# Performance work log

Measured on AMD Instinct MI355X. Metric: run time of the kernel, lower is better.

## Reference

```python
import jax, jax.numpy as jnp
import numpy as np

B, S, D_IN, D_OUT, H = 2, 2048, 1024, 1024, 16
HD = D_OUT // H


def setup_inputs() -> dict:
    key = jax.random.key(0)
    ks = jax.random.split(key, 6)
    x = jax.random.normal(ks[0], (B, S, D_IN), jnp.float32)
    Wq = jax.random.normal(ks[1], (D_IN, D_OUT), jnp.float32) * 0.02
    Wk = jax.random.normal(ks[2], (D_IN, D_OUT), jnp.float32) * 0.02
    Wv = jax.random.normal(ks[3], (D_IN, D_OUT), jnp.float32) * 0.02
    Wo = jax.random.normal(ks[4], (D_OUT, D_OUT), jnp.float32) * 0.02
    bo = jax.random.normal(ks[5], (D_OUT,), jnp.float32) * 0.02
    return {"x": x, "Wq": Wq, "Wk": Wk, "Wv": Wv, "Wo": Wo, "bo": bo}


def reference(x, Wq, Wk, Wv, Wo, bo):
    b, s, _ = x.shape

    def to_heads(t):  # [b, s, d_out] -> [b, h, s, hd]
        return t.reshape(b, s, H, HD).transpose(0, 2, 1, 3)

    Q = to_heads(x @ Wq)
    K = to_heads(x @ Wk)
    V = to_heads(x @ Wv)

    scale = 1.0 / jnp.sqrt(jnp.asarray(HD, x.dtype))
    scores = jnp.einsum("bhqd,bhkd->bhqk", Q, K) * scale
    causal_mask = jnp.triu(jnp.ones((s, s), dtype=bool), k=1)  # True above diag
    scores = jnp.where(causal_mask, jnp.asarray(-1e6, scores.dtype), scores)
    weights = jax.nn.softmax(scores, axis=-1)  # dropout p=0.0 -> identity
    attn = jnp.einsum("bhqk,bhkd->bhqd", weights, V)  # [b, h, s, hd]
    # Faithful to source: reshape [b,h,s,hd] -> [b,s,d_out] WITHOUT head transpose-back
    attn = attn.reshape(b, s, D_OUT)
    return attn @ Wo + bo
```

## Files before the change

kernel.cpp:

```cpp
#include <hip/hip_runtime.h>
#include <stdint.h>


typedef unsigned short u16;
typedef __attribute__((ext_vector_type(8))) short bf16x8;
typedef __attribute__((ext_vector_type(4))) float f32x4;

#define MFMA_BF16(a, b, c) __builtin_amdgcn_mfma_f32_16x16x32_bf16((a), (b), (c), 0, 0, 0)
#define QSCALE 0.18033688011112042f

#if __has_builtin(__builtin_amdgcn_exp2f)
#define EXP2(x) __builtin_amdgcn_exp2f(x)
#else
#define EXP2(x) exp2f(x)
#endif

__device__ __forceinline__ u16 f2bf(float f) {
  union { float f; unsigned int u; } x; x.f = f;
  unsigned int r = x.u + 0x7fffu + ((x.u >> 16) & 1u);
  return (u16)(r >> 16);
}
__device__ __forceinline__ bf16x8 pack8(float4 a, float4 b) {
  bf16x8 r;
  r[0] = (short)f2bf(a.x); r[1] = (short)f2bf(a.y);
  r[2] = (short)f2bf(a.z); r[3] = (short)f2bf(a.w);
  r[4] = (short)f2bf(b.x); r[5] = (short)f2bf(b.y);
  r[6] = (short)f2bf(b.z); r[7] = (short)f2bf(b.w);
  return r;
}
__device__ __forceinline__ void gload_lds16(const u16* g, u16* l) {
  __builtin_amdgcn_global_load_lds((__attribute__((address_space(1))) void*)g,
                                   (__attribute__((address_space(3))) void*)l, 16, 0, 0);
}

template <int CPR>
__device__ __forceinline__ int sw_off(int r, int c) {
  return (r * CPR + (c ^ (r & (CPR - 1)))) * 8;
}

__global__ __launch_bounds__(1024) void prep(
    const float* __restrict__ x, u16* __restrict__ xb,
    const float* __restrict__ Wq, const float* __restrict__ Wk,
    const float* __restrict__ Wv, const float* __restrict__ Wo,
    u16* __restrict__ WoT, u16* __restrict__ WT3) {
  const int bxg = blockIdx.x, by = blockIdx.y;
  if (bxg >= 128) {
    const int blk = (bxg - 128) * 32 + by;
    const int tid = threadIdx.y * 32 + threadIdx.x;
    const size_t i = ((size_t)blk * 1024 + tid) * 8;
    const float4 a = *(const float4*)&x[i];
    const float4 b2 = *(const float4*)&x[i + 4];
    *(bf16x8*)&xb[i] = pack8(a, b2);
    return;
  }
  __shared__ u16 t[32][33];
  const float* W;
  u16* T;
  int j0, wcol;
  if (bxg < 32) {
    j0 = bxg * 32; wcol = j0; W = Wo; T = WoT;
  } else {
    j0 = (bxg - 32) * 32;
    const int g = j0 >> 10;
    W = (g == 0) ? Wq : (g == 1) ? Wk : Wv;
    T = WT3;
    wcol = j0 & 1023;
  }
  const int k0 = by * 32;
  t[threadIdx.y][threadIdx.x] =
      f2bf(W[(size_t)(k0 + threadIdx.y) * 1024 + wcol + threadIdx.x]);
  __syncthreads();
  T[(size_t)(j0 + threadIdx.y) * 1024 + k0 + threadIdx.x] = t[threadIdx.x][threadIdx.y];
}

__global__ __launch_bounds__(256) void x_to_bf16(const float* __restrict__ x,
                                                 u16* __restrict__ xb) {
  const size_t i = ((size_t)blockIdx.x * 256 + threadIdx.x) * 8;
  const float4 a = *(const float4*)&x[i];
  const float4 b = *(const float4*)&x[i + 4];
  *(bf16x8*)&xb[i] = pack8(a, b);
}

__global__ void transpose_cols(const float* __restrict__ W0, const float* __restrict__ W1,
                               const float* __restrict__ W2, u16* __restrict__ T,
                               int h0, int hsx64) {
  __shared__ u16 t[32][33];
  const int j0 = blockIdx.x * 32;
  const int g = j0 / hsx64;
  const float* W = (g == 0) ? W0 : (g == 1) ? W1 : W2;
  const int wc0 = h0 * 64 + (j0 % hsx64);
  const int k0 = blockIdx.y * 32;
  t[threadIdx.y][threadIdx.x] =
      f2bf(W[(size_t)(k0 + threadIdx.y) * 1024 + wc0 + threadIdx.x]);
  __syncthreads();
  T[(size_t)(j0 + threadIdx.y) * 1024 + k0 + threadIdx.x] = t[threadIdx.x][threadIdx.y];
}

template <int MODE, int AF32>
__global__ __launch_bounds__(256, 2) void gemm_bt(
    const void* __restrict__ Av, const u16* __restrict__ BT,
    void* __restrict__ C0v, u16* __restrict__ C1, u16* __restrict__ C2,
    const float* __restrict__ bias, int M, int N, int K, int hs, int h0) {
  __shared__ __align__(16) u16 lsA[2][128 * 32];
  __shared__ __align__(16) u16 lsB[2][128 * 32];
  const int tid = threadIdx.x, lane = tid & 63, wv = tid >> 6;
  const int quad = lane >> 4, l16 = lane & 15;
  const int m0 = blockIdx.y * 128, n0 = blockIdx.x * 128;
  const int wm = (wv >> 1) * 64, wn = (wv & 1) * 64;
  const int hs64 = hs * 64;
  f32x4 acc[4][4] = {};

  if constexpr (!AF32) {
#pragma unroll
    for (int c = 0; c < 2; ++c) {
      const int P = c * 256 + tid, r = P >> 2;
      const int gcol = ((P & 3) ^ (r & 3)) * 8;
      gload_lds16((const u16*)Av + (size_t)(m0 + r) * K + gcol,
                  &lsA[0][(c * 256 + wv * 64) * 8]);
      gload_lds16(BT + (size_t)(n0 + r) * K + gcol,
                  &lsB[0][(c * 256 + wv * 64) * 8]);
    }
    __syncthreads();
    const int nk = K >> 5;
    for (int kt = 0; kt < nk; ++kt) {
      const int buf = kt & 1;
      if (kt + 1 < nk) {
        const int k1 = (kt + 1) << 5;
#pragma unroll
        for (int c = 0; c < 2; ++c) {
          const int P = c * 256 + tid, r = P >> 2;
          const int gcol = ((P & 3) ^ (r & 3)) * 8;
          gload_lds16((const u16*)Av + (size_t)(m0 + r) * K + k1 + gcol,
                      &lsA[buf ^ 1][(c * 256 + wv * 64) * 8]);
          gload_lds16(BT + (size_t)(n0 + r) * K + k1 + gcol,
                      &lsB[buf ^ 1][(c * 256 + wv * 64) * 8]);
        }
      }
      bf16x8 af[4], bfr[4];
#pragma unroll
      for (int i = 0; i < 4; ++i)
        af[i] = *(const bf16x8*)&lsA[buf][sw_off<4>(wm + i * 16 + l16, quad)];
#pragma unroll
      for (int j = 0; j < 4; ++j)
        bfr[j] = *(const bf16x8*)&lsB[buf][sw_off<4>(wn + j * 16 + l16, quad)];
#pragma unroll
      for (int i = 0; i < 4; ++i)
#pragma unroll
        for (int j = 0; j < 4; ++j) acc[i][j] = MFMA_BF16(af[i], bfr[j], acc[i][j]);
      __syncthreads();
    }
  } else {
    for (int k0 = 0; k0 < K; k0 += 32) {
      bf16x8 va[2], vb[2];
#pragma unroll
      for (int c = 0; c < 2; ++c) {
        const int P = c * 256 + tid, r = P >> 2, cc = P & 3;
        const float* Af = (const float*)Av;
        const float4 a0 = *(const float4*)&Af[(size_t)(m0 + r) * K + k0 + cc * 8];
        const float4 a1 = *(const float4*)&Af[(size_t)(m0 + r) * K + k0 + cc * 8 + 4];
        va[c] = pack8(a0, a1);
        vb[c] = *(const bf16x8*)&BT[(size_t)(n0 + r) * K + k0 + cc * 8];
      }
      __syncthreads();
#pragma unroll
      for (int c = 0; c < 2; ++c) {
        const int P = c * 256 + tid, r = P >> 2, cc = P & 3;
        *(bf16x8*)&lsA[0][sw_off<4>(r, cc)] = va[c];
        *(bf16x8*)&lsB[0][sw_off<4>(r, cc)] = vb[c];
      }
      __syncthreads();
      bf16x8 af[4], bfr[4];
#pragma unroll
      for (int i = 0; i < 4; ++i)
        af[i] = *(const bf16x8*)&lsA[0][sw_off<4>(wm + i * 16 + l16, quad)];
#pragma unroll
      for (int j = 0; j < 4; ++j)
        bfr[j] = *(const bf16x8*)&lsB[0][sw_off<4>(wn + j * 16 + l16, quad)];
#pragma unroll
      for (int i = 0; i < 4; ++i)
#pragma unroll
        for (int j = 0; j < 4; ++j) acc[i][j] = MFMA_BF16(af[i], bfr[j], acc[i][j]);
    }
  }

  if constexpr (MODE == 3) {
#pragma unroll
    for (int j = 0; j < 4; ++j) {
      const int n = n0 + wn + j * 16 + l16;
#pragma unroll
      for (int i = 0; i < 4; ++i) {
        const int mb = m0 + wm + i * 16 + quad * 4;
        const int b = mb >> 11, s0 = mb & 2047;
        if (n < hs64) {
#pragma unroll
          for (int r = 0; r < 4; ++r)
            ((u16*)C0v)[((size_t)b * 2048 + s0 + r) * hs64 + n] =
                f2bf(acc[i][j][r] * QSCALE);
        } else if (n < 2 * hs64) {
#pragma unroll
          for (int r = 0; r < 4; ++r)
            C1[((size_t)b * 2048 + s0 + r) * hs64 + (n - hs64)] = f2bf(acc[i][j][r]);
        } else {
          const int nn = n - 2 * hs64;
          uint2 o;
          o.x = (unsigned)f2bf(acc[i][j][0]) | ((unsigned)f2bf(acc[i][j][1]) << 16);
          o.y = (unsigned)f2bf(acc[i][j][2]) | ((unsigned)f2bf(acc[i][j][3]) << 16);
          *(uint2*)&C2[((size_t)(b * hs + (nn >> 6)) * 64 + (nn & 63)) * 2048 + s0] = o;
        }
      }
    }
  } else {
#pragma unroll
    for (int i = 0; i < 4; ++i)
#pragma unroll
      for (int j = 0; j < 4; ++j) {
        const int n = n0 + wn + j * 16 + l16;
        float bv = 0.f;
        if constexpr (MODE == 1) bv = bias[n];
#pragma unroll
        for (int r = 0; r < 4; ++r) {
          const int m = m0 + wm + i * 16 + quad * 4 + r;
          const int b = (m >= hs * 128) ? 1 : 0;
          const int rp = m - b * hs * 128;
          ((float*)C0v)[(size_t)(b * 2048 + h0 * 128 + rp) * 1024 + n] =
              acc[i][j][r] + bv;
        }
      }
  }
}

__global__ __launch_bounds__(256, 2) void attn_fwd(
    const u16* __restrict__ Qsl, const u16* __restrict__ Ksl,
    const u16* __restrict__ VTsl, u16* __restrict__ A2sl, int hs) {
  __shared__ __align__(16) u16 lsK[3][64 * 64];
  __shared__ __align__(16) u16 lsV[3][64 * 64];
  __shared__ __align__(16) u16 lsP[4][16 * 64];
  __shared__ __align__(16) float scrl[64];
  const int tid = threadIdx.x, lane = tid & 63, wv = tid >> 6;
  const int quad = lane >> 4, l16 = lane & 15;
  const int grp = wv >> 1, wq = wv & 1;

  const int cpx = gridDim.x >> 3;
  const int w = (blockIdx.x & 7) * cpx + (blockIdx.x >> 3);
  const int bh = w >> 4, bx = w & 15;

  const int b = (bh >= hs) ? 1 : 0, hh = bh - b * hs;
  const int hs64 = hs * 64;
  const u16* Qb = Qsl + (size_t)b * 2048 * hs64;
  const u16* Kb = Ksl + (size_t)b * 2048 * hs64;
  const u16* Vb = VTsl + (size_t)(b * hs + hh) * 64 * 2048;
  u16* A2b = A2sl + (size_t)(b * hs + hh) * 2048 * 64;
  u16* lsPw = &lsP[wv][0];
  float* scro = (float*)&lsK[0][0];

  bf16x8 ones;
#pragma unroll
  for (int i = 0; i < 8; ++i) ones[i] = (short)0x3F80;

  const int prow = l16 >> 1;
  const int pb0 = (l16 & 1) << 2;

  const int Pa = tid, ra = Pa >> 3, ca = (Pa & 7) ^ (ra & 7);
  const int Pb2 = 256 + tid, rb = Pb2 >> 3, cb = (Pb2 & 7) ^ (rb & 7);
  const size_t kTileStep = (size_t)64 * hs64;
  const u16* const kBa = Kb + (size_t)ra * hs64 + hh * 64 + ca * 8;
  const u16* const kBb = Kb + (size_t)rb * hs64 + hh * 64 + cb * 8;
  const u16* const vBa = Vb + (size_t)ra * 2048 + ca * 8;
  const u16* const vBb = Vb + (size_t)rb * 2048 + cb * 8;
  const int dA = (wv * 64) * 8;
  const int dB = (256 + wv * 64) * 8;

  for (int half = 0; half < 2; ++half) {
    const int qt = (half == 0) ? bx : 31 - bx;
    const int q0 = qt * 64;

    bf16x8 qf[2][2];
#pragma unroll
    for (int j = 0; j < 2; ++j)
#pragma unroll
      for (int ks = 0; ks < 2; ++ks)
        qf[j][ks] = *(const bf16x8*)&Qb[(size_t)(q0 + wq * 32 + j * 16 + l16) * hs64 +
                                        hh * 64 + ks * 32 + quad * 8];

    f32x4 acc_o[2][4] = {};
    f32x4 acc_l[2] = {};

    const u16* pkA = kBa;
    const u16* pkB = kBb;
    const u16* pvA = vBa;
    const u16* pvB = vBb;
    int bc = 0, bn = 1, bf_ = 2;

    auto stage = [&](int bs) {
      gload_lds16(pkA, &lsK[bs][dA]);
      gload_lds16(pkB, &lsK[bs][dB]);
      gload_lds16(pvA, &lsV[bs][dA]);
      gload_lds16(pvB, &lsV[bs][dB]);
      pkA += kTileStep; pkB += kTileStep; pvA += 64; pvB += 64;
    };
    auto qk = [&](int bK, f32x4 (&S)[2][2]) {
#pragma unroll
      for (int j = 0; j < 2; ++j)
#pragma unroll
        for (int nj = 0; nj < 2; ++nj) S[j][nj] = f32x4{0.f, 0.f, 0.f, 0.f};
#pragma unroll
      for (int ks = 0; ks < 2; ++ks)
#pragma unroll
        for (int nj = 0; nj < 2; ++nj) {
          const bf16x8 kf = *(const bf16x8*)
              &lsK[bK][sw_off<8>(grp * 32 + nj * 16 + l16, ks * 4 + quad)];
          S[0][nj] = MFMA_BF16(kf, qf[0][ks], S[0][nj]);
          S[1][nj] = MFMA_BF16(kf, qf[1][ks], S[1][nj]);
        }
    };
    auto smpv = [&](f32x4 (&S)[2][2], int bV, bool domask) {
#pragma unroll
      for (int j = 0; j < 2; ++j) {
        const int grow = wq * 32 + j * 16 + l16;
#pragma unroll
        for (int nj = 0; nj < 2; ++nj) {
#pragma unroll
          for (int r = 0; r < 4; ++r) {
            float p = EXP2(S[j][nj][r]);
            if (domask) {
              const int keyb = grp * 32 + nj * 16 + quad * 4;
              p = (keyb + r > grow) ? 0.f : p;
            }
            S[j][nj][r] = p;
          }
          union { float f; unsigned int u; } t0, t1, t2, t3;
          t0.f = S[j][nj][0]; t1.f = S[j][nj][1];
          t2.f = S[j][nj][2]; t3.f = S[j][nj][3];
          uint2 wpk;
          wpk.x = (t0.u >> 16) | (t1.u & 0xFFFF0000u);
          wpk.y = (t2.u >> 16) | (t3.u & 0xFFFF0000u);
          const int row = j * 8 + prow;
          const int chunk = (pb0 + 2 * nj + (quad >> 1)) ^ prow;
          *(uint2*)&lsPw[row * 64 + chunk * 8 + (quad & 1) * 4] = wpk;
        }
      }
      bf16x8 pf[2];
#pragma unroll
      for (int j = 0; j < 2; ++j) {
        const int row = j * 8 + prow;
        const int chunk = (pb0 + quad) ^ prow;
        pf[j] = *(const bf16x8*)&lsPw[row * 64 + chunk * 8];
        acc_l[j] = MFMA_BF16(ones, pf[j], acc_l[j]);
      }
#pragma unroll
      for (int njo = 0; njo < 4; ++njo) {
        const bf16x8 vf = *(const bf16x8*)
            &lsV[bV][sw_off<8>(njo * 16 + l16, grp * 4 + quad)];
        acc_o[0][njo] = MFMA_BF16(vf, pf[0], acc_o[0][njo]);
        acc_o[1][njo] = MFMA_BF16(vf, pf[1], acc_o[1][njo]);
      }
    };
    auto step = [&](f32x4 (&Sc)[2][2], f32x4 (&Sn)[2][2], int kt) {
      __syncthreads();
      if (kt + 2 <= qt) stage(bf_);
      qk(bn, Sn);
      smpv(Sc, bc, false);
      const int t = bc; bc = bn; bn = bf_; bf_ = t;
    };

    __syncthreads();
    stage(0);
    __syncthreads();
    if (qt >= 1) stage(1);

    f32x4 sA[2][2], sB[2][2];
    qk(0, sA);

    int kt = 0;
    while (kt + 1 < qt) { step(sA, sB, kt); step(sB, sA, kt + 1); kt += 2; }
    bool curA = true;
    if (kt < qt) { step(sA, sB, kt); curA = false; }
    if (curA) smpv(sA, bc, true); else smpv(sB, bc, true);

    __syncthreads();
    if (grp == 1) {
#pragma unroll
      for (int j = 0; j < 2; ++j) {
#pragma unroll
        for (int njo = 0; njo < 4; ++njo) {
          const int ch = (njo * 4 + quad) ^ l16;
          *(f32x4*)&scro[(size_t)(wq * 32 + j * 16 + l16) * 64 + ch * 4] =
              acc_o[j][njo];
        }
        if (quad == 0) scrl[wq * 32 + j * 16 + l16] = acc_l[j][0];
      }
    }
    __syncthreads();
    if (grp == 0) {
#pragma unroll
      for (int j = 0; j < 2; ++j) {
        const int ql = wq * 32 + j * 16 + l16;
        const float inv = 1.0f / (acc_l[j][0] + scrl[ql]);
#pragma unroll
        for (int njo = 0; njo < 4; ++njo) {
          const int ch = (njo * 4 + quad) ^ l16;
          const f32x4 ob = *(const f32x4*)&scro[(size_t)ql * 64 + ch * 4];
          uint2 o;
          o.x = (unsigned)f2bf((acc_o[j][njo][0] + ob[0]) * inv) |
                ((unsigned)f2bf((acc_o[j][njo][1] + ob[1]) * inv) << 16);
          o.y = (unsigned)f2bf((acc_o[j][njo][2] + ob[2]) * inv) |
                ((unsigned)f2bf((acc_o[j][njo][3] + ob[3]) * inv) << 16);
          *(uint2*)&A2b[(size_t)(q0 + ql) * 64 + njo * 16 + quad * 4] = o;
        }
      }
    }
  }
}

extern "C" void kernel_launch(void* const* d_in, const int* in_sizes, int n_in,
                              void* d_out, int out_size, void* d_ws, size_t ws_size,
                              hipStream_t stream) {
  (void)in_sizes; (void)n_in; (void)out_size;
  const float* x  = (const float*)d_in[0];
  const float* Wq = (const float*)d_in[1];
  const float* Wk = (const float*)d_in[2];
  const float* Wv = (const float*)d_in[3];
  const float* Wo = (const float*)d_in[4];
  const float* bo = (const float*)d_in[5];
  float* out = (float*)d_out;
  char* ws = (char*)d_ws;
  const size_t MB = 1024 * 1024;
  const size_t KB = 1024;

  int hs = 2;
  if      (ws_size >= 2 * MB + 16 * 2432 * KB) hs = 16;
  else if (ws_size >= 2 * MB +  8 * 2432 * KB) hs = 8;
  else if (ws_size >= 2 * MB +  4 * 2432 * KB) hs = 4;

  u16* WoT   = (u16*)(ws);
  u16* Ksl   = (u16*)(ws + 2 * MB);
  u16* VTsl  = (u16*)(ws + 2 * MB + (size_t)hs *  512 * KB);
  u16* A2sl  = (u16*)(ws + 2 * MB + (size_t)hs * 1024 * KB);
  u16* WT3sl = (u16*)(ws + 2 * MB + (size_t)hs * 1536 * KB);
  u16* Qsl   = (u16*)(ws + 2 * MB + (size_t)hs * 1920 * KB);

  if (hs == 16) {
    u16* xb = A2sl;
    prep<<<dim3(144, 32), dim3(32, 32), 0, stream>>>(x, xb, Wq, Wk, Wv, Wo, WoT, WT3sl);
    gemm_bt<3, 0><<<dim3(24, 32), 256, 0, stream>>>(
        (const void*)xb, WT3sl, (void*)Qsl, Ksl, VTsl, nullptr, 4096, 3072, 1024, 16, 0);
    attn_fwd<<<dim3(512), 256, 0, stream>>>(Qsl, Ksl, VTsl, A2sl, 16);
    gemm_bt<1, 0><<<dim3(8, 32), 256, 0, stream>>>(
        (const void*)A2sl, WoT, (void*)out, nullptr, nullptr, bo, 4096, 1024, 1024, 16, 0);
  } else {
    transpose_cols<<<dim3(32, 32), dim3(32, 32), 0, stream>>>(Wo, Wo, Wo, WoT, 0, 1024);
    for (int h0 = 0; h0 < 16; h0 += hs) {
      transpose_cols<<<dim3(6 * hs, 32), dim3(32, 32), 0, stream>>>(Wq, Wk, Wv, WT3sl, h0, hs * 64);
      gemm_bt<3, 1><<<dim3((3 * hs) / 2, 32), 256, 0, stream>>>(
          (const void*)x, WT3sl, (void*)Qsl, Ksl, VTsl, nullptr, 4096, 3 * hs * 64, 1024, hs, h0);
      attn_fwd<<<dim3(16 * 2 * hs), 256, 0, stream>>>(Qsl, Ksl, VTsl, A2sl, hs);
      gemm_bt<1, 0><<<dim3(8, 2 * hs), 256, 0, stream>>>(
          (const void*)A2sl, WoT, (void*)out, nullptr, nullptr, bo, 2 * hs * 128, 1024, 1024, hs, h0);
    }
  }
}
```

Measured before the change: 179.5 us.

## Deepen bf16 GEMM LDS pipeline to four stages with explicit vmcnt waits

Moves the bf16-A GEMM path from a double-buffered LDS pipeline to a 4-buffer ring with three tiles of direct global-to-LDS loads in flight. Each iteration waits only until the current tile has landed, using explicit s_waitcnt vmcnt counts, then synchronises with a single barrier per iteration. The goal is to hide global memory latency better. It doubles LDS use to 64 KB per block, which may lower occupancy under launch_bounds(256,2), and it relies on the vmcnt counting being exact.

Result: slower. 194.0 us (+8.0%).

```diff
diff --git a/kernel.cpp b/kernel.cpp
--- a/kernel.cpp
+++ b/kernel.cpp
@@ -101,8 +101,8 @@
     const void* __restrict__ Av, const u16* __restrict__ BT,
     void* __restrict__ C0v, u16* __restrict__ C1, u16* __restrict__ C2,
     const float* __restrict__ bias, int M, int N, int K, int hs, int h0) {
-  __shared__ __align__(16) u16 lsA[2][128 * 32];
-  __shared__ __align__(16) u16 lsB[2][128 * 32];
+  __shared__ __align__(16) u16 lsA[4][128 * 32];
+  __shared__ __align__(16) u16 lsB[4][128 * 32];
   const int tid = threadIdx.x, lane = tid & 63, wv = tid >> 6;
   const int quad = lane >> 4, l16 = lane & 15;
   const int m0 = blockIdx.y * 128, n0 = blockIdx.x * 128;
@@ -111,31 +111,35 @@
   f32x4 acc[4][4] = {};
 
   if constexpr (!AF32) {
-#pragma unroll
-    for (int c = 0; c < 2; ++c) {
-      const int P = c * 256 + tid, r = P >> 2;
-      const int gcol = ((P & 3) ^ (r & 3)) * 8;
-      gload_lds16((const u16*)Av + (size_t)(m0 + r) * K + gcol,
-                  &lsA[0][(c * 256 + wv * 64) * 8]);
-      gload_lds16(BT + (size_t)(n0 + r) * K + gcol,
-                  &lsB[0][(c * 256 + wv * 64) * 8]);
-    }
-    __syncthreads();
     const int nk = K >> 5;
+    const int P0 = tid, r0 = P0 >> 2, g0 = ((P0 & 3) ^ (r0 & 3)) * 8;
+    const int P1 = 256 + tid, r1 = P1 >> 2, g1 = ((P1 & 3) ^ (r1 & 3)) * 8;
+    const u16* const A0 = (const u16*)Av + (size_t)(m0 + r0) * K + g0;
+    const u16* const A1 = (const u16*)Av + (size_t)(m0 + r1) * K + g1;
+    const u16* const B0 = BT + (size_t)(n0 + r0) * K + g0;
+    const u16* const B1 = BT + (size_t)(n0 + r1) * K + g1;
+    const int d0 = (wv * 64) * 8, d1 = (256 + wv * 64) * 8;
+
+    auto stage = [&](int kt, int bb) {
+      const int k0 = kt << 5;
+      gload_lds16(A0 + k0, &lsA[bb][d0]);
+      gload_lds16(A1 + k0, &lsA[bb][d1]);
+      gload_lds16(B0 + k0, &lsB[bb][d0]);
+      gload_lds16(B1 + k0, &lsB[bb][d1]);
+    };
+
+    stage(0, 0);
+    if (nk > 1) stage(1, 1);
+    if (nk > 2) stage(2, 2);
+
     for (int kt = 0; kt < nk; ++kt) {
-      const int buf = kt & 1;
-      if (kt + 1 < nk) {
-        const int k1 = (kt + 1) << 5;
-#pragma unroll
-        for (int c = 0; c < 2; ++c) {
-          const int P = c * 256 + tid, r = P >> 2;
-          const int gcol = ((P & 3) ^ (r & 3)) * 8;
-          gload_lds16((const u16*)Av + (size_t)(m0 + r) * K + k1 + gcol,
-                      &lsA[buf ^ 1][(c * 256 + wv * 64) * 8]);
-          gload_lds16(BT + (size_t)(n0 + r) * K + k1 + gcol,
-                      &lsB[buf ^ 1][(c * 256 + wv * 64) * 8]);
-        }
-      }
+      if (kt < nk - 2)       asm volatile("s_waitcnt vmcnt(8)" ::: "memory");
+      else if (kt == nk - 2) asm volatile("s_waitcnt vmcnt(4)" ::: "memory");
+      else                   asm volatile("s_waitcnt vmcnt(0)" ::: "memory");
+      __builtin_amdgcn_s_barrier();
+      __builtin_amdgcn_sched_barrier(0);
+      if (kt + 3 < nk) stage(kt + 3, (kt + 3) & 3);
+      const int buf = kt & 3;
       bf16x8 af[4], bfr[4];
 #pragma unroll
       for (int i = 0; i < 4; ++i)
@@ -147,7 +151,6 @@
       for (int i = 0; i < 4; ++i)
 #pragma unroll
         for (int j = 0; j < 4; ++j) acc[i][j] = MFMA_BF16(af[i], bfr[j], acc[i][j]);
-      __syncthreads();
     }
   } else {
     for (int k0 = 0; k0 < K; k0 += 32) {
```
